# Kernel tuning notes

Measured on AMD Instinct MI355X. Metric: run time of the kernel, lower is better.

## Reference

```python
import jax, jax.numpy as jnp
import numpy as np

HID = 5120
H = 40
DN = 128   # qk_nope_head_dim
DR = 64    # qk_rope_head_dim
DQK = DN + DR
DV = 128   # v_head_dim
QLR = 1536 # q_lora_rank
KVLR = 512 # kv_lora_rank
EPS = 1e-6
ROPE_THETA = 10000.0


def setup_inputs() -> dict:
    key = jax.random.key(0)
    ks = jax.random.split(key, 8)
    B, S = 2, 2048
    s = 0.02
    return {
        "x": jax.random.normal(ks[0], (B, S, HID), dtype=jnp.float32),
        # fused down-projection: q_lora + kv_lora + k_pe
        "w_a": jax.random.normal(ks[1], (HID, QLR + KVLR + DR), dtype=jnp.float32) * s,
        "q_ln_w": jnp.ones((QLR,), dtype=jnp.float32),
        "kv_ln_w": jnp.ones((KVLR,), dtype=jnp.float32),
        "w_qb": jax.random.normal(ks[2], (QLR, H * DQK), dtype=jnp.float32) * s,
        "w_kvb": jax.random.normal(ks[3], (KVLR, H * (DN + DV)), dtype=jnp.float32) * s,
        "w_o": jax.random.normal(ks[4], (H * DV, HID), dtype=jnp.float32) * s,
    }


def _rmsnorm(x, w):
    var = jnp.mean(jnp.square(x), axis=-1, keepdims=True)
    return x * jax.lax.rsqrt(var + EPS) * w


def _rope_cos_sin(S, dtype):
    half = DR // 2
    inv_freq = 1.0 / (ROPE_THETA ** (jnp.arange(half, dtype=jnp.float32) / half))
    ang = jnp.arange(S, dtype=jnp.float32)[:, None] * inv_freq[None, :]  # [S, half]
    return jnp.cos(ang).astype(dtype), jnp.sin(ang).astype(dtype)


def _apply_rope(t, cos, sin):
    # t: [..., S, h, DR]; cos/sin: [S, DR/2]
    t1, t2 = jnp.split(t, 2, axis=-1)
    c = cos[None, :, None, :]
    s = sin[None, :, None, :]
    return jnp.concatenate([t1 * c - t2 * s, t2 * c + t1 * s], axis=-1)


def mla_forward(x, w_a, q_ln_w, kv_ln_w, w_qb, w_kvb, w_o):
    B, S, _ = x.shape
    # fused low-rank down-projection
    a = x @ w_a  # [B, S, QLR + KVLR + DR]
    q_c = _rmsnorm(a[..., :QLR], q_ln_w)
    kv_c = _rmsnorm(a[..., QLR:QLR + KVLR], kv_ln_w)
    k_pe = a[..., QLR + KVLR:]  # [B, S, DR] shared across heads (MQA-style)

    q = (q_c @ w_qb).reshape(B, S, H, DQK)
    q_nope, q_pe = q[..., :DN], q[..., DN:]
    kv = (kv_c @ w_kvb).reshape(B, S, H, DN + DV)
    k_nope, v = kv[..., :DN], kv[..., DN:]

    cos, sin = _rope_cos_sin(S, x.dtype)
    q_pe = _apply_rope(q_pe, cos, sin)                  # [B,S,H,DR]
    k_pe = _apply_rope(k_pe[:, :, None, :], cos, sin)    # [B,S,1,DR]

    qh = jnp.concatenate([q_nope, q_pe], axis=-1)                                 # [B,S,H,DQK]
    kh = jnp.concatenate([k_nope, jnp.broadcast_to(k_pe, (B, S, H, DR))], axis=-1)  # [B,S,H,DQK]

    scale = 1.0 / np.sqrt(DQK)
    scores = jnp.einsum('bqhd,bkhd->bhqk', qh, kh) * scale
    causal = jnp.tril(jnp.ones((S, S), dtype=bool))
    scores = jnp.where(causal[None, None], scores, jnp.finfo(scores.dtype).min)
    attn = jax.nn.softmax(scores, axis=-1)
    o = jnp.einsum('bhqk,bkhd->bqhd', attn, v).reshape(B, S, H * DV)
    return o @ w_o


def reference(x, w_a, q_ln_w, kv_ln_w, w_qb, w_kvb, w_o):
    return mla_forward(x, w_a, q_ln_w, kv_ln_w, w_qb, w_kvb, w_o)
```

## Files before the change

kernel.cpp:

```cpp
#include <hip/hip_runtime.h>

typedef unsigned short u16;
typedef __attribute__((ext_vector_type(8))) short bf16x8;
typedef __attribute__((ext_vector_type(4))) float f32x4;

__device__ __forceinline__ float bf2f(u16 u) {
  unsigned int x = ((unsigned int)u) << 16;
  return __builtin_bit_cast(float, x);
}
__device__ __forceinline__ u16 f2bf(float f) {
  unsigned int x = __builtin_bit_cast(unsigned int, f);
  x += 0x7fff + ((x >> 16) & 1);
  return (u16)(x >> 16);
}
__device__ __forceinline__ void gload16(const u16* g, u16* l) {
  __builtin_amdgcn_global_load_lds((const __attribute__((address_space(1))) void*)g,
                                   (__attribute__((address_space(3))) void*)l, 16, 0, 0);
}
#define MFMA16(a, b, c) __builtin_amdgcn_mfma_f32_16x16x32_bf16(a, b, c, 0, 0, 0)

__global__ __launch_bounds__(256) void convert_k(const float* __restrict__ in,
                                                 u16* __restrict__ out, int n4) {
  const int i = blockIdx.x * 256 + threadIdx.x;
  if (i < n4) {
    float4 f = ((const float4*)in)[i];
    ushort4 v;
    v.x = f2bf(f.x); v.y = f2bf(f.y); v.z = f2bf(f.z); v.w = f2bf(f.w);
    ((ushort4*)out)[i] = v;
  }
}

__global__ __launch_bounds__(256) void transpose_k(const float* __restrict__ in,
                                                   u16* __restrict__ out,
                                                   int R, int C) {
  __shared__ u16 t[64][65];
  const int r0 = blockIdx.x * 64, c0 = blockIdx.y * 64;
  const int x = threadIdx.x & 15, y = threadIdx.x >> 4;
  if (c0 < C) {
#pragma unroll
    for (int i = 0; i < 4; i++) {
      const float* g = in + (size_t)(r0 + y + 16 * i) * C + c0 + 4 * x;
      float4 v = *(const float4*)g;
      t[y + 16 * i][4 * x + 0] = f2bf(v.x);
      t[y + 16 * i][4 * x + 1] = f2bf(v.y);
      t[y + 16 * i][4 * x + 2] = f2bf(v.z);
      t[y + 16 * i][4 * x + 3] = f2bf(v.w);
    }
    __syncthreads();
#pragma unroll
    for (int i = 0; i < 4; i++) {
      const int cc = y + 16 * i;
      ushort4 v;
      v.x = t[4 * x + 0][cc];
      v.y = t[4 * x + 1][cc];
      v.z = t[4 * x + 2][cc];
      v.w = t[4 * x + 3][cc];
      *(ushort4*)(out + (size_t)(c0 + cc) * R + r0 + 4 * x) = v;
    }
  } else {
    ushort4 z = {0, 0, 0, 0};
#pragma unroll
    for (int i = 0; i < 4; i++)
      *(ushort4*)(out + (size_t)(c0 + y + 16 * i) * R + r0 + 4 * x) = z;
  }
}

template <int MODE>
__global__ __launch_bounds__(256) void gemm_bt(const u16* __restrict__ A, int lda,
                                               const u16* __restrict__ Bt, int ldb,
                                               void* __restrict__ Cp, int ldc,
                                               u16* __restrict__ C1, int K) {
  __shared__ u16 lA[128 * 32];
  __shared__ u16 lB[128 * 32];
  const int tid = threadIdx.x;
  const int m0 = blockIdx.x * 128, n0 = blockIdx.y * 128;
  const int w = tid >> 6, lane = tid & 63, r = lane & 15, quad = lane >> 4;
  const int wr = (w >> 1) * 64, wc = (w & 1) * 64;

  f32x4 acc[4][4];
#pragma unroll
  for (int i = 0; i < 4; i++)
#pragma unroll
    for (int j = 0; j < 4; j++) acc[i][j] = (f32x4){0.f, 0.f, 0.f, 0.f};

  const int r_a = tid >> 2;
  const int c_a = (tid & 3) * 8;
  const u16* gA = A + (size_t)(m0 + r_a) * lda + c_a;
  const u16* gB = Bt + (size_t)(n0 + r_a) * ldb + c_a;
  u16* lAb = lA + (tid & 192) * 8;
  u16* lBb = lB + (tid & 192) * 8;

  for (int k0 = 0; k0 < K; k0 += 32) {
    __syncthreads();
    gload16(gA + k0, lAb);
    gload16(gA + (size_t)64 * lda + k0, lAb + 2048);
    gload16(gB + k0, lBb);
    gload16(gB + (size_t)64 * ldb + k0, lBb + 2048);
    __syncthreads();
    bf16x8 af[4], bf[4];
#pragma unroll
    for (int i = 0; i < 4; i++) af[i] = *(const bf16x8*)&lA[(wr + i * 16 + r) * 32 + quad * 8];
#pragma unroll
    for (int j = 0; j < 4; j++) bf[j] = *(const bf16x8*)&lB[(wc + j * 16 + r) * 32 + quad * 8];
#pragma unroll
    for (int i = 0; i < 4; i++)
#pragma unroll
      for (int j = 0; j < 4; j++) acc[i][j] = MFMA16(af[i], bf[j], acc[i][j]);
  }

#pragma unroll
  for (int i = 0; i < 4; i++) {
#pragma unroll
    for (int j = 0; j < 4; j++) {
#pragma unroll
      for (int reg = 0; reg < 4; reg++) {
        const int row = m0 + wr + i * 16 + quad * 4 + reg;
        const int col = n0 + wc + j * 16 + r;
        const float fv = acc[i][j][reg];
        if (MODE == 0) {
          ((u16*)Cp)[(size_t)row * ldc + col] = f2bf(fv);
        } else if (MODE == 2) {
          ((float*)Cp)[(size_t)row * ldc + col] = fv;
        } else {
          const int hh = col >> 8, cc = col & 255;
          if (cc < 128) {
            ((u16*)Cp)[(size_t)row * 5120 + hh * 128 + cc] = f2bf(fv);
          } else {
            const int bb = row >> 11, ss = row & 2047;
            C1[(((size_t)(bb * 40 + hh)) * 128 + (cc - 128)) * 2048 + ss] = f2bf(fv);
          }
        }
      }
    }
  }
}

__global__ __launch_bounds__(256) void rmsnorm_k(u16* __restrict__ a,
                                                 const float* __restrict__ qw,
                                                 const float* __restrict__ kvw) {
  const int row = blockIdx.x, seg = blockIdx.y;
  const int off = seg ? 1536 : 0;
  const int width = seg ? 512 : 1536;
  const float* wp = seg ? kvw : qw;
  u16* p = a + (size_t)row * 2176 + off;
  const int tid = threadIdx.x;
  float ss = 0.f;
  for (int i = tid; i < width; i += 256) {
    float v = bf2f(p[i]);
    ss += v * v;
  }
#pragma unroll
  for (int o = 32; o >= 1; o >>= 1) ss += __shfl_xor(ss, o, 64);
  __shared__ float red[4];
  if ((tid & 63) == 0) red[tid >> 6] = ss;
  __syncthreads();
  const float tot = red[0] + red[1] + red[2] + red[3];
  const float rs = rsqrtf(tot / (float)width + 1e-6f);
  for (int i = tid; i < width; i += 256) p[i] = f2bf(bf2f(p[i]) * rs * wp[i]);
}

__global__ __launch_bounds__(256) void rope_k(u16* __restrict__ a, u16* __restrict__ q) {
  const int row = blockIdx.x;
  const int s = row & 2047;
  const int tid = threadIdx.x;
  __shared__ float cs[32], sn[32];
  if (tid < 32) {
    float inv = powf(10000.f, -(float)tid * (1.f / 32.f));
    float ang = (float)s * inv;
    cs[tid] = cosf(ang);
    sn[tid] = sinf(ang);
  }
  __syncthreads();
  if (tid < 32) {
    u16* p = a + (size_t)row * 2176 + 2048;
    float t1 = bf2f(p[tid]), t2 = bf2f(p[tid + 32]);
    p[tid] = f2bf(t1 * cs[tid] - t2 * sn[tid]);
    p[tid + 32] = f2bf(t2 * cs[tid] + t1 * sn[tid]);
  }
  for (int item = tid; item < 1280; item += 256) {
    const int hh = item >> 5, i = item & 31;
    u16* p = q + (size_t)row * 7680 + hh * 192 + 128;
    float t1 = bf2f(p[i]), t2 = bf2f(p[i + 32]);
    p[i] = f2bf(t1 * cs[i] - t2 * sn[i]);
    p[i + 32] = f2bf(t2 * cs[i] + t1 * sn[i]);
  }
}

__global__ __launch_bounds__(256) void attn_k(const u16* __restrict__ q,
                                              const u16* __restrict__ kn,
                                              const u16* __restrict__ aB,
                                              const u16* __restrict__ vT,
                                              u16* __restrict__ o) {
  __shared__ u16 lK[6 * 64 * 32];
  __shared__ u16 lV[2 * 128 * 32];
  __shared__ u16 lP[4][16 * 72];
  const int qt = blockIdx.x, h = blockIdx.y, b = blockIdx.z;
  const int q0 = qt * 64;
  const int tid = threadIdx.x, w = tid >> 6, lane = tid & 63, r = lane & 15, quad = lane >> 4;
  const int srow = tid >> 2, sseg = tid & 3;
  const int wbase = (tid & 192) * 8;

  bf16x8 qf[6];
  {
    const u16* qrow = q + (((size_t)(b * 2048 + q0 + w * 16 + r)) * 40 + h) * 192;
#pragma unroll
    for (int kd = 0; kd < 6; kd++) qf[kd] = *(const bf16x8*)(qrow + kd * 32 + quad * 8);
  }
  f32x4 oa[8];
#pragma unroll
  for (int f = 0; f < 8; f++) oa[f] = (f32x4){0.f, 0.f, 0.f, 0.f};
  float m_i[4], l_i[4];
#pragma unroll
  for (int t = 0; t < 4; t++) {
    m_i[t] = -3.0e38f;
    l_i[t] = 0.f;
  }
  u16* lPw = lP[w];

  for (int kt = 0; kt <= qt; kt++) {
    const int k0 = kt * 64;
    __syncthreads();
#pragma unroll
    for (int kd = 0; kd < 6; kd++) {
      const u16* g =
          (kd < 4)
              ? kn + (((size_t)(b * 2048 + k0 + srow)) * 40 + h) * 128 + kd * 32 + sseg * 8
              : aB + ((size_t)(b * 2048 + k0 + srow)) * 2176 + 2048 + (kd - 4) * 32 + sseg * 8;
      gload16(g, &lK[kd * 2048 + wbase]);
    }
#pragma unroll
    for (int it = 0; it < 4; it++) {
      const int ks = it >> 1, half = it & 1;
      const u16* g = vT + (((size_t)(b * 40 + h)) * 128 + half * 64 + srow) * 2048 +
                     k0 + ks * 32 + sseg * 8;
      gload16(g, &lV[ks * 4096 + half * 2048 + wbase]);
    }
    __syncthreads();

    f32x4 s[4];
#pragma unroll
    for (int j = 0; j < 4; j++) s[j] = (f32x4){0.f, 0.f, 0.f, 0.f};
#pragma unroll
    for (int kd = 0; kd < 6; kd++) {
#pragma unroll
      for (int j = 0; j < 4; j++) {
        bf16x8 bk = *(const bf16x8*)&lK[kd * 2048 + (j * 16 + r) * 32 + quad * 8];
        s[j] = MFMA16(qf[kd], bk, s[j]);
      }
    }
    const float sc = 0.0721687836487032f;
    const bool diag = (kt == qt);
    float mc[4];
#pragma unroll
    for (int t = 0; t < 4; t++) {
      float mx = -3.0e38f;
#pragma unroll
      for (int j = 0; j < 4; j++) {
        float v = s[j][t] * sc;
        if (diag && (j * 16 + r > w * 16 + quad * 4 + t)) v = -3.0e38f;
        s[j][t] = v;
        mx = fmaxf(mx, v);
      }
      mc[t] = mx;
    }
#pragma unroll
    for (int off = 1; off < 16; off <<= 1) {
#pragma unroll
      for (int t = 0; t < 4; t++) mc[t] = fmaxf(mc[t], __shfl_xor(mc[t], off, 64));
    }
    float al[4], ls[4];
#pragma unroll
    for (int t = 0; t < 4; t++) {
      const float mn = fmaxf(m_i[t], mc[t]);
      al[t] = __expf(m_i[t] - mn);
      m_i[t] = mn;
      float sum = 0.f;
#pragma unroll
      for (int j = 0; j < 4; j++) {
        float pv = __expf(s[j][t] - mn);
        s[j][t] = pv;
        sum += pv;
      }
      ls[t] = sum;
    }
#pragma unroll
    for (int off = 1; off < 16; off <<= 1) {
#pragma unroll
      for (int t = 0; t < 4; t++) ls[t] += __shfl_xor(ls[t], off, 64);
    }
#pragma unroll
    for (int t = 0; t < 4; t++) l_i[t] = l_i[t] * al[t] + ls[t];
#pragma unroll
    for (int f = 0; f < 8; f++)
#pragma unroll
      for (int t = 0; t < 4; t++) oa[f][t] *= al[t];
#pragma unroll
    for (int t = 0; t < 4; t++)
#pragma unroll
      for (int j = 0; j < 4; j++) lPw[(quad * 4 + t) * 72 + j * 16 + r] = f2bf(s[j][t]);
#pragma unroll
    for (int ks = 0; ks < 2; ks++) {
      bf16x8 ap = *(const bf16x8*)&lPw[r * 72 + ks * 32 + quad * 8];
#pragma unroll
      for (int f = 0; f < 8; f++) {
        bf16x8 bv = *(const bf16x8*)&lV[ks * 4096 + (f * 16 + r) * 32 + quad * 8];
        oa[f] = MFMA16(ap, bv, oa[f]);
      }
    }
  }
#pragma unroll
  for (int t = 0; t < 4; t++) {
    const float inv = 1.0f / l_i[t];
    u16* op = o + ((size_t)(b * 2048 + q0 + w * 16 + quad * 4 + t)) * 5120 + h * 128;
#pragma unroll
    for (int f = 0; f < 8; f++) op[f * 16 + r] = f2bf(oa[f][t] * inv);
  }
}

extern "C" void kernel_launch(void* const* d_in, const int* in_sizes, int n_in,
                              void* d_out, int out_size, void* d_ws, size_t ws_size,
                              hipStream_t stream) {
  const float* x = (const float*)d_in[0];
  const float* w_a = (const float*)d_in[1];
  const float* qlw = (const float*)d_in[2];
  const float* kvlw = (const float*)d_in[3];
  const float* w_qb = (const float*)d_in[4];
  const float* w_kvb = (const float*)d_in[5];
  const float* w_o = (const float*)d_in[6];
  float* out = (float*)d_out;

  char* base = (char*)d_ws;
  u16* aB   = (u16*)(base);
  u16* qB   = (u16*)(base + 17825792ULL);
  u16* knop = (u16*)(base + 80740352ULL);
  u16* vT   = (u16*)(base + 122683392ULL);
  u16* xB   = (u16*)(base + 164626432ULL);
  u16* waT  = (u16*)(base + 206569472ULL);
  u16* wqbT = (u16*)(base + 164626432ULL);
  u16* wkvT = (u16*)(base + 164626432ULL);
  u16* woT  = (u16*)(base + 164626432ULL);
  u16* oB   = (u16*)(base + 217055232ULL);

  convert_k<<<20480, 256, 0, stream>>>(x, xB, 5242880);
  transpose_k<<<dim3(5120 / 64, 2176 / 64), 256, 0, stream>>>(w_a, waT, 5120, 2112);
  gemm_bt<0><<<dim3(32, 17), 256, 0, stream>>>(xB, 5120, waT, 5120, aB, 2176, nullptr, 5120);
  rmsnorm_k<<<dim3(4096, 2), 256, 0, stream>>>(aB, qlw, kvlw);
  transpose_k<<<dim3(1536 / 64, 7680 / 64), 256, 0, stream>>>(w_qb, wqbT, 1536, 7680);
  gemm_bt<0><<<dim3(32, 60), 256, 0, stream>>>(aB, 2176, wqbT, 1536, qB, 7680, nullptr, 1536);
  transpose_k<<<dim3(512 / 64, 10240 / 64), 256, 0, stream>>>(w_kvb, wkvT, 512, 10240);
  gemm_bt<1><<<dim3(32, 80), 256, 0, stream>>>(aB + 1536, 2176, wkvT, 512, knop, 0, vT, 512);
  transpose_k<<<dim3(5120 / 64, 5120 / 64), 256, 0, stream>>>(w_o, woT, 5120, 5120);
  rope_k<<<4096, 256, 0, stream>>>(aB, qB);
  attn_k<<<dim3(32, 40, 2), 256, 0, stream>>>(qB, knop, aB, vT, oB);
  gemm_bt<2><<<dim3(32, 40), 256, 0, stream>>>(oB, 5120, woT, 5120, out, 5120, nullptr, 5120);
}
```

Before: 1.556 ms.

## Double-buffer attention K/V tiles with smaller key blocks and per-wave causal skip

Restructures the attention kernel to stage 32-key K/V tiles into double-buffered LDS, so the next tile's global-to-LDS load overlaps compute on the current one, with one barrier per iteration. It also reverses the query-tile launch order so the heaviest causal blocks start first. Each wave skips key tiles that lie fully above its causal diagonal, rescales the accumulator only when some row's max grows, and raises wave priority around the MFMA sections. In exchange there are twice as many loop iterations with more per-tile softmax overhead, and per-wave branching.

```diff
diff --git a/kernel.cpp b/kernel.cpp
--- a/kernel.cpp
+++ b/kernel.cpp
@@ -191,14 +191,13 @@
                                               const u16* __restrict__ aB,
                                               const u16* __restrict__ vT,
                                               u16* __restrict__ o) {
-  __shared__ u16 lK[6 * 64 * 32];
-  __shared__ u16 lV[2 * 128 * 32];
-  __shared__ u16 lP[4][16 * 72];
-  const int qt = blockIdx.x, h = blockIdx.y, b = blockIdx.z;
+  __shared__ u16 lK[2][6 * 32 * 32];
+  __shared__ u16 lV[2][128 * 32];
+  __shared__ u16 lP[4][16 * 36];
+  const int qt = (int)gridDim.x - 1 - blockIdx.x, h = blockIdx.y, b = blockIdx.z;
   const int q0 = qt * 64;
   const int tid = threadIdx.x, w = tid >> 6, lane = tid & 63, r = lane & 15, quad = lane >> 4;
-  const int srow = tid >> 2, sseg = tid & 3;
-  const int wbase = (tid & 192) * 8;
+  const int srow = lane >> 2, sseg = (lane & 3) * 8;
 
   bf16x8 qf[6];
   {
@@ -216,97 +215,122 @@
     l_i[t] = 0.f;
   }
   u16* lPw = lP[w];
-
-  for (int kt = 0; kt <= qt; kt++) {
-    const int k0 = kt * 64;
-    __syncthreads();
-#pragma unroll
-    for (int kd = 0; kd < 6; kd++) {
+  const int nkt = 2 * (qt + 1);
+
+  auto stage = [&](int bufi, int kt) {
+    const int k0 = kt * 32;
+    u16* lKb = lK[bufi];
+    u16* lVb = lV[bufi];
+#pragma unroll
+    for (int c = w; c < 12; c += 4) {
+      const int kd = c >> 1;
+      const int row = (c & 1) * 16 + srow;
       const u16* g =
           (kd < 4)
-              ? kn + (((size_t)(b * 2048 + k0 + srow)) * 40 + h) * 128 + kd * 32 + sseg * 8
-              : aB + ((size_t)(b * 2048 + k0 + srow)) * 2176 + 2048 + (kd - 4) * 32 + sseg * 8;
-      gload16(g, &lK[kd * 2048 + wbase]);
-    }
-#pragma unroll
-    for (int it = 0; it < 4; it++) {
-      const int ks = it >> 1, half = it & 1;
-      const u16* g = vT + (((size_t)(b * 40 + h)) * 128 + half * 64 + srow) * 2048 +
-                     k0 + ks * 32 + sseg * 8;
-      gload16(g, &lV[ks * 4096 + half * 2048 + wbase]);
+              ? kn + (((size_t)(b * 2048 + k0 + row)) * 40 + h) * 128 + kd * 32 + sseg
+              : aB + ((size_t)(b * 2048 + k0 + row)) * 2176 + 2048 + (kd - 4) * 32 + sseg;
+      gload16(g, lKb + c * 512 + lane * 8);
+    }
+#pragma unroll
+    for (int c = w; c < 8; c += 4) {
+      const int row = c * 16 + srow;
+      const u16* g = vT + (((size_t)(b * 40 + h)) * 128 + row) * 2048 + k0 + sseg;
+      gload16(g, lVb + c * 512 + lane * 8);
+    }
+  };
+
+  stage(0, 0);
+  __syncthreads();
+
+  for (int kt = 0; kt < nkt; kt++) {
+    const int k0 = kt * 32;
+    if (kt + 1 < nkt) stage((kt + 1) & 1, kt + 1);
+    const u16* lKb = lK[kt & 1];
+    const u16* lVb = lV[kt & 1];
+    if (k0 <= q0 + w * 16 + 15) {
+      f32x4 s[2];
+      s[0] = (f32x4){0.f, 0.f, 0.f, 0.f};
+      s[1] = (f32x4){0.f, 0.f, 0.f, 0.f};
+      __builtin_amdgcn_s_setprio(1);
+#pragma unroll
+      for (int kd = 0; kd < 6; kd++) {
+#pragma unroll
+        for (int j = 0; j < 2; j++) {
+          bf16x8 bk = *(const bf16x8*)&lKb[kd * 1024 + (j * 16 + r) * 32 + quad * 8];
+          s[j] = MFMA16(qf[kd], bk, s[j]);
+        }
+      }
+      __builtin_amdgcn_s_setprio(0);
+      const float sc = 0.0721687836487032f;
+      const bool diag = (k0 + 31 > q0 + w * 16);
+      const int kq = k0 + r - q0 - w * 16 - quad * 4;
+      float mc[4];
+#pragma unroll
+      for (int t = 0; t < 4; t++) {
+        float mx = -3.0e38f;
+#pragma unroll
+        for (int j = 0; j < 2; j++) {
+          float v = s[j][t] * sc;
+          if (diag && (kq + j * 16 > t)) v = -3.0e38f;
+          s[j][t] = v;
+          mx = fmaxf(mx, v);
+        }
+        mc[t] = mx;
+      }
+#pragma unroll
+      for (int off = 1; off < 16; off <<= 1) {
+#pragma unroll
+        for (int t = 0; t < 4; t++) mc[t] = fmaxf(mc[t], __shfl_xor(mc[t], off, 64));
+      }
+      bool grow = false;
+#pragma unroll
+      for (int t = 0; t < 4; t++) grow = grow || (mc[t] > m_i[t]);
+      if (__any(grow)) {
+#pragma unroll
+        for (int t = 0; t < 4; t++) {
+          const float mn = fmaxf(m_i[t], mc[t]);
+          const float al = __expf(m_i[t] - mn);
+          m_i[t] = mn;
+          l_i[t] *= al;
+#pragma unroll
+          for (int f = 0; f < 8; f++) oa[f][t] *= al;
+        }
+      }
+      float ls[4];
+#pragma unroll
+      for (int t = 0; t < 4; t++) {
+        float sum = 0.f;
+#pragma unroll
+        for (int j = 0; j < 2; j++) {
+          float pv = __expf(s[j][t] - m_i[t]);
+          s[j][t] = pv;
+          sum += pv;
+        }
+        ls[t] = sum;
+      }
+#pragma unroll
+      for (int off = 1; off < 16; off <<= 1) {
+#pragma unroll
+        for (int t = 0; t < 4; t++) ls[t] += __shfl_xor(ls[t], off, 64);
+      }
+#pragma unroll
+      for (int t = 0; t < 4; t++) l_i[t] += ls[t];
+#pragma unroll
+      for (int t = 0; t < 4; t++) {
+#pragma unroll
+        for (int j = 0; j < 2; j++)
+          lPw[(quad * 4 + t) * 36 + j * 16 + r] = f2bf(s[j][t]);
+      }
+      bf16x8 ap = *(const bf16x8*)&lPw[r * 36 + quad * 8];
+      __builtin_amdgcn_s_setprio(1);
+#pragma unroll
+      for (int f = 0; f < 8; f++) {
+        bf16x8 bv = *(const bf16x8*)&lVb[(f * 16 + r) * 32 + quad * 8];
+        oa[f] = MFMA16(ap, bv, oa[f]);
+      }
+      __builtin_amdgcn_s_setprio(0);
     }
     __syncthreads();
-
-    f32x4 s[4];
-#pragma unroll
-    for (int j = 0; j < 4; j++) s[j] = (f32x4){0.f, 0.f, 0.f, 0.f};
-#pragma unroll
-    for (int kd = 0; kd < 6; kd++) {
-#pragma unroll
-      for (int j = 0; j < 4; j++) {
-        bf16x8 bk = *(const bf16x8*)&lK[kd * 2048 + (j * 16 + r) * 32 + quad * 8];
-        s[j] = MFMA16(qf[kd], bk, s[j]);
-      }
-    }
-    const float sc = 0.0721687836487032f;
-    const bool diag = (kt == qt);
-    float mc[4];
-#pragma unroll
-    for (int t = 0; t < 4; t++) {
-      float mx = -3.0e38f;
-#pragma unroll
-      for (int j = 0; j < 4; j++) {
-        float v = s[j][t] * sc;
-        if (diag && (j * 16 + r > w * 16 + quad * 4 + t)) v = -3.0e38f;
-        s[j][t] = v;
-        mx = fmaxf(mx, v);
-      }
-      mc[t] = mx;
-    }
-#pragma unroll
-    for (int off = 1; off < 16; off <<= 1) {
-#pragma unroll
-      for (int t = 0; t < 4; t++) mc[t] = fmaxf(mc[t], __shfl_xor(mc[t], off, 64));
-    }
-    float al[4], ls[4];
-#pragma unroll
-    for (int t = 0; t < 4; t++) {
-      const float mn = fmaxf(m_i[t], mc[t]);
-      al[t] = __expf(m_i[t] - mn);
-      m_i[t] = mn;
-      float sum = 0.f;
-#pragma unroll
-      for (int j = 0; j < 4; j++) {
-        float pv = __expf(s[j][t] - mn);
-        s[j][t] = pv;
-        sum += pv;
-      }
-      ls[t] = sum;
-    }
-#pragma unroll
-    for (int off = 1; off < 16; off <<= 1) {
-#pragma unroll
-      for (int t = 0; t < 4; t++) ls[t] += __shfl_xor(ls[t], off, 64);
-    }
-#pragma unroll
-    for (int t = 0; t < 4; t++) l_i[t] = l_i[t] * al[t] + ls[t];
-#pragma unroll
-    for (int f = 0; f < 8; f++)
-#pragma unroll
-      for (int t = 0; t < 4; t++) oa[f][t] *= al[t];
-#pragma unroll
-    for (int t = 0; t < 4; t++)
-#pragma unroll
-      for (int j = 0; j < 4; j++) lPw[(quad * 4 + t) * 72 + j * 16 + r] = f2bf(s[j][t]);
-#pragma unroll
-    for (int ks = 0; ks < 2; ks++) {
-      bf16x8 ap = *(const bf16x8*)&lPw[r * 72 + ks * 32 + quad * 8];
-#pragma unroll
-      for (int f = 0; f < 8; f++) {
-        bf16x8 bv = *(const bf16x8*)&lV[ks * 4096 + (f * 16 + r) * 32 + quad * 8];
-        oa[f] = MFMA16(ap, bv, oa[f]);
-      }
-    }
   }
 #pragma unroll
   for (int t = 0; t < 4; t++) {
```

Result: slower. 1.667 ms (+7.1%).
